# Optimization experiments

Measured on AMD Instinct MI355X. Metric: run time of the kernel, lower is better.

Reference implementation:

```python
import jax, jax.numpy as jnp
import numpy as np

B, CIN, H, W = 8, 128, 64, 64
COUT, KH, KW = 128, 3, 3
STRIDE = (1, 1)
PAD = (1, 1)
DIL = (1, 1)
GROUPS = 1
OFFSET_GROUPS = 1

def _out_size(i, k, s, p, d):
    return (i + 2 * p - d * (k - 1) - 1) // s + 1

HO = _out_size(H, KH, STRIDE[0], PAD[0], DIL[0])
WO = _out_size(W, KW, STRIDE[1], PAD[1], DIL[1])


def setup_inputs() -> dict:
    key = jax.random.key(0)
    k1, k2, k3, k4 = jax.random.split(key, 4)
    x = jax.random.normal(k1, (B, CIN, H, W), jnp.float32)
    offset = jax.random.normal(k2, (B, 2 * OFFSET_GROUPS * KH * KW, HO, WO), jnp.float32)
    fan_in = (CIN // GROUPS) * KH * KW
    bound = 1.0 / np.sqrt(fan_in)
    weight = jax.random.uniform(k3, (COUT, CIN // GROUPS, KH, KW), jnp.float32, -bound, bound)
    bias = jax.random.uniform(k4, (COUT,), jnp.float32, -bound, bound)
    return {"x": x, "offset": offset, "weight": weight, "bias": bias}


def _deform_conv2d(x, offset, weight, bias):
    Bn, Cin, Hi, Wi = x.shape
    K = KH * KW
    Goff, Gw = OFFSET_GROUPS, GROUPS
    Cpg = Cin // Goff

    # base sampling positions (before learned offsets)
    ys = jnp.arange(HO, dtype=jnp.float32) * STRIDE[0] - PAD[0]  # [HO]
    xs = jnp.arange(WO, dtype=jnp.float32) * STRIDE[1] - PAD[1]  # [WO]
    base_y = jnp.repeat(jnp.arange(KH, dtype=jnp.float32) * DIL[0], KW)  # [K]
    base_x = jnp.tile(jnp.arange(KW, dtype=jnp.float32) * DIL[1], KH)    # [K]

    # offsets: channel layout is 2*(g*K + k) + {0: dy, 1: dx}
    off = offset.reshape(Bn, Goff, K, 2, HO, WO)
    py = base_y[None, None, :, None, None] + ys[None, None, None, :, None] + off[:, :, :, 0]  # [B,Goff,K,HO,WO]
    px = base_x[None, None, :, None, None] + xs[None, None, None, None, :] + off[:, :, :, 1]

    y0 = jnp.floor(py)
    x0 = jnp.floor(px)
    ly = py - y0  # fractional weights
    lx = px - x0

    xg = x.reshape(Bn, Goff, Cpg, Hi * Wi)

    def gather_one(img, lin):  # img [Cpg, H*W], lin [K,HO,WO] -> [Cpg,K,HO,WO]
        return img[:, lin]

    gather = jax.vmap(jax.vmap(gather_one))  # over B and Goff

    def corner(yi, xi, w):
        # zero-padding semantics: out-of-bounds corner contributes 0
        mask = (yi >= 0) & (yi < Hi) & (xi >= 0) & (xi < Wi)
        iy = jnp.clip(yi, 0, Hi - 1).astype(jnp.int32)
        ix = jnp.clip(xi, 0, Wi - 1).astype(jnp.int32)
        lin = iy * Wi + ix  # [B,Goff,K,HO,WO]
        wm = (w * mask.astype(x.dtype))[:, :, None]  # broadcast over channel axis
        return gather(xg, lin) * wm  # [B,Goff,Cpg,K,HO,WO]

    val = (corner(y0, x0, (1 - ly) * (1 - lx))
           + corner(y0, x0 + 1, (1 - ly) * lx)
           + corner(y0 + 1, x0, ly * (1 - lx))
           + corner(y0 + 1, x0 + 1, ly * lx))  # [B,Goff,Cpg,K,HO,WO]

    # grouped conv accumulate
    val = val.reshape(Bn, Gw, Cin // Gw, K, HO, WO)
    wg = weight.reshape(Gw, COUT // Gw, Cin // Gw, K)
    out = jnp.einsum('bgckhw,gock->bgohw', val, wg).reshape(Bn, COUT, HO, WO)
    return out + bias[None, :, None, None]


def reference(x, offset, weight, bias):
    return _deform_conv2d(x, offset, weight, bias)
```

## Files before the change

kernel.cpp:

```cpp
#include <hip/hip_runtime.h>

typedef unsigned int   u32;
typedef unsigned short u16;
typedef short bf16x8 __attribute__((ext_vector_type(8)));
typedef float f32x4  __attribute__((ext_vector_type(4)));
typedef float f32x2  __attribute__((ext_vector_type(2)));

#define CIN   128
#define COUT  128
#define Hh    64
#define Ww    64
#define Bb    8
#define NKSTEP 36
#define XT_ELEMS (Bb*Hh*Ww*CIN)

__device__ __forceinline__ float bflo(u32 u){ return __uint_as_float(u << 16); }
__device__ __forceinline__ float bfhi(u32 u){ return __uint_as_float(u & 0xffff0000u); }

__device__ __forceinline__ u32 pack2(float a, float b){
    u32 lo = __float_as_uint(a) + 0x8000u;
    u32 hi = __float_as_uint(b) + 0x8000u;
    return __builtin_amdgcn_perm(hi, lo, 0x07060302u);
}
__device__ __forceinline__ u16 tobf(float a){
    u32 ua = __float_as_uint(a);
    ua += 0x7fffu + ((ua >> 16) & 1u);
    return (u16)(ua >> 16);
}

__global__ __launch_bounds__(256) void k_transpose(const float* __restrict__ x,
                                                   u16* __restrict__ xT){
    __shared__ float lds[64*132];
    int bi = blockIdx.x;
    int hb = bi & 63, b = bi >> 6;
    int tid = threadIdx.x;

    {
        int r = tid >> 1, cq = tid & 1;
        const float* xp = x + ((size_t)(b*128 + r))*4096 + hb*64 + cq*32;
        float4 v[8];
#pragma unroll
        for (int k = 0; k < 8; ++k) v[k] = *(const float4*)(xp + k*4);
        float* dst = lds + (cq*32)*132 + r;
#pragma unroll
        for (int k = 0; k < 8; ++k){
            dst[(k*4+0)*132] = v[k].x;
            dst[(k*4+1)*132] = v[k].y;
            dst[(k*4+2)*132] = v[k].z;
            dst[(k*4+3)*132] = v[k].w;
        }
    }
    __syncthreads();
    {
        int s = tid >> 2, kq = tid & 3;
        const float* src = lds + s*132 + kq*32;
        u32 r16[16];
#pragma unroll
        for (int k = 0; k < 8; ++k){
            float4 v = *(const float4*)(src + k*4);
            r16[k*2  ] = pack2(v.x, v.y);
            r16[k*2+1] = pack2(v.z, v.w);
        }
        u32* dst = (u32*)xT + ((size_t)(b*4096 + hb*64 + s))*64 + kq*16;
#pragma unroll
        for (int k = 0; k < 4; ++k)
            *(uint4*)(dst + k*4) = *(uint4*)&r16[k*4];
    }
}

__global__ __launch_bounds__(256) void k_wprep(const float* __restrict__ w,
                                               u16* __restrict__ Wt){
    int gid = blockIdx.x*256 + threadIdx.x;
    int jf   = gid & 7;
    int lane = (gid >> 3) & 63;
    int mt   = (gid >> 9) & 7;
    int kt   = gid >> 12;
    int m  = mt*16 + (lane & 15);
    int kk = (lane >> 4)*8 + jf;
    int ck = kt*32 + kk;
    int kpos = ck >> 7;
    int cin  = ck & 127;
    Wt[gid] = tobf(w[((size_t)m*128 + cin)*9 + kpos]);
}

__global__ __launch_bounds__(256, 4)
void k_main(const float* __restrict__ off, const float* __restrict__ bias,
            const u16* __restrict__ xT, const u16* __restrict__ Wt,
            float* __restrict__ out){
    __shared__ u32 Vsm[2][32*20];

    int tid = threadIdx.x;
    int bi  = blockIdx.x;
    int b   = bi & 7;
    int t   = bi >> 3;
    int s0  = t * 32;
    int ho  = s0 >> 6, wo0 = s0 & 63;

    int p = tid >> 3, o = tid & 7;
    int wo = wo0 + p;
    const u16* xb = xT + (size_t)b * (Hh*Ww*CIN);

    int lane = tid & 63, wave = tid >> 6;
    int wm = wave >> 1, wn = wave & 1;
    int quad = lane >> 4, l16 = lane & 15;

    f32x4 acc[4];
#pragma unroll
    for (int i = 0; i < 4; ++i) acc[i] = {0.f, 0.f, 0.f, 0.f};

    int   aa[4];
    float wt[4];

    auto state = [&](int kpos){
        int kh = kpos / 3, kw = kpos - kh*3;
        size_t ob = ((size_t)(b*18 + 2*kpos))*4096 + (s0 + p);
        float dy = off[ob];
        float dx = off[ob + 4096];
        float py = (float)(ho + kh - 1) + dy;
        float px = (float)(wo + kw - 1) + dx;
        float y0f = floorf(py), x0f = floorf(px);
        float ly = py - y0f, lx = px - x0f;
        int y0 = (int)y0f, x0 = (int)x0f;
        int y1 = y0 + 1,  x1 = x0 + 1;
        float my0 = (y0 >= 0 && y0 < Hh) ? 1.f : 0.f;
        float my1 = (y1 >= 0 && y1 < Hh) ? 1.f : 0.f;
        float mx0 = (x0 >= 0 && x0 < Ww) ? 1.f : 0.f;
        float mx1 = (x1 >= 0 && x1 < Ww) ? 1.f : 0.f;
        float oy = 1.f - ly, ox = 1.f - lx;
        wt[0] = oy*ox*my0*mx0;
        wt[1] = oy*lx*my0*mx1;
        wt[2] = ly*ox*my1*mx0;
        wt[3] = ly*lx*my1*mx1;
        int cy0 = min(max(y0,0),Hh-1), cy1 = min(max(y1,0),Hh-1);
        int cx0 = min(max(x0,0),Ww-1), cx1 = min(max(x1,0),Ww-1);
        aa[0] = (cy0*Ww + cx0)*CIN;
        aa[1] = (cy0*Ww + cx1)*CIN;
        aa[2] = (cy1*Ww + cx0)*CIN;
        aa[3] = (cy1*Ww + cx1)*CIN;
    };

    auto gather = [&](int ks, uint2 q[4]){
        int coff = ((ks & 3) << 5) + o*4;
        const u16* xc = xb + coff;
#pragma unroll
        for (int c = 0; c < 4; ++c)
            q[c] = *(const uint2*)(xc + aa[c]);
    };

    auto loadA = [&](int ks, uint4 a[4]){
        const u16* wp = Wt + (size_t)((ks*8 + wm*4)*64 + lane)*8;
#pragma unroll
        for (int i = 0; i < 4; ++i)
            a[i] = *(const uint4*)(wp + (size_t)i*64*8);
    };

    auto blend_store = [&](const uint2 q[4], int buf){
        u32 r2[2];
#pragma unroll
        for (int d = 0; d < 2; ++d){
            f32x2 s = {0.f, 0.f};
#pragma unroll
            for (int c = 0; c < 4; ++c){
                u32 u = ((const u32*)q)[c*2 + d];
                f32x2 v  = { bflo(u), bfhi(u) };
                f32x2 w2 = { wt[c], wt[c] };
                s += w2 * v;
            }
            r2[d] = pack2(s.x, s.y);
        }
        *(uint2*)&Vsm[buf][p*20 + o*2] = *(uint2*)&r2[0];
    };

    uint2 q[4];
    uint4 araw_cur[4], araw_nxt[4];
    state(0);
    gather(0, q);
    loadA(0, araw_cur);
    blend_store(q, 0);

    for (int ks = 0; ks < NKSTEP; ++ks){
        __syncthreads();
        int nxt = ks + 1;
        bool have_nxt = (nxt < NKSTEP);
        if (have_nxt){
            if ((nxt & 3) == 0) state(nxt >> 2);
            gather(nxt, q);
            loadA(nxt, araw_nxt);
        }

        uint4 braw = *(const uint4*)&Vsm[ks & 1][(wn*16 + l16)*20 + quad*4];
        bf16x8 bv = __builtin_bit_cast(bf16x8, braw);
#pragma unroll
        for (int i = 0; i < 4; ++i){
            bf16x8 av = __builtin_bit_cast(bf16x8, araw_cur[i]);
            acc[i] = __builtin_amdgcn_mfma_f32_16x16x32_bf16(av, bv, acc[i], 0, 0, 0);
        }

        if (have_nxt){
            blend_store(q, nxt & 1);
#pragma unroll
            for (int i = 0; i < 4; ++i) araw_cur[i] = araw_nxt[i];
        }
    }

    int pcol = wn*16 + l16;
#pragma unroll
    for (int i = 0; i < 4; ++i){
        int cout0 = (wm*4 + i)*16 + quad*4;
        size_t obase = ((size_t)(b*COUT + cout0))*4096 + (s0 + pcol);
#pragma unroll
        for (int r = 0; r < 4; ++r)
            out[obase + (size_t)r*4096] = acc[i][r] + bias[cout0 + r];
    }
}

extern "C" void kernel_launch(void* const* d_in, const int* in_sizes, int n_in,
                              void* d_out, int out_size, void* d_ws, size_t ws_size,
                              hipStream_t stream){
    const float* x    = (const float*)d_in[0];
    const float* off  = (const float*)d_in[1];
    const float* w    = (const float*)d_in[2];
    const float* bias = (const float*)d_in[3];
    float* out = (float*)d_out;

    u16* xT = (u16*)d_ws;
    u16* Wt = xT + XT_ELEMS;

    k_transpose<<<dim3(512),  dim3(256), 0, stream>>>(x, xT);
    k_wprep    <<<dim3(576),  dim3(256), 0, stream>>>(w, Wt);
    k_main     <<<dim3(1024), dim3(256), 0, stream>>>(off, bias, xT, Wt, out);
}
```

Measured before the change: 119.7 us.

## Deepen gather pipeline to two steps ahead and prefetch offsets

```diff
diff --git a/kernel.cpp b/kernel.cpp
--- a/kernel.cpp
+++ b/kernel.cpp
@@ -99,6 +99,7 @@
     int p = tid >> 3, o = tid & 7;
     int wo = wo0 + p;
     const u16* xb = xT + (size_t)b * (Hh*Ww*CIN);
+    const float* offp = off + ((size_t)b*18)*4096 + s0 + p;
 
     int lane = tid & 63, wave = tid >> 6;
     int wm = wave >> 1, wn = wave & 1;
@@ -108,14 +109,19 @@
 #pragma unroll
     for (int i = 0; i < 4; ++i) acc[i] = {0.f, 0.f, 0.f, 0.f};
 
-    int   aa[4];
-    float wt[4];
-
-    auto state = [&](int kpos){
+    int   aaS[2][4];
+    float wtS[2][4];
+    float dyN, dxN;
+
+    auto load_off = [&](int kpos){
+        const float* op = offp + (size_t)(2*kpos)*4096;
+        dyN = op[0];
+        dxN = op[4096];
+    };
+    auto state = [&](int kpos, int st){
+        float dy = dyN, dx = dxN;
+        if (kpos < 8) load_off(kpos + 1);
         int kh = kpos / 3, kw = kpos - kh*3;
-        size_t ob = ((size_t)(b*18 + 2*kpos))*4096 + (s0 + p);
-        float dy = off[ob];
-        float dx = off[ob + 4096];
         float py = (float)(ho + kh - 1) + dy;
         float px = (float)(wo + kw - 1) + dx;
         float y0f = floorf(py), x0f = floorf(px);
@@ -127,34 +133,31 @@
         float mx0 = (x0 >= 0 && x0 < Ww) ? 1.f : 0.f;
         float mx1 = (x1 >= 0 && x1 < Ww) ? 1.f : 0.f;
         float oy = 1.f - ly, ox = 1.f - lx;
-        wt[0] = oy*ox*my0*mx0;
-        wt[1] = oy*lx*my0*mx1;
-        wt[2] = ly*ox*my1*mx0;
-        wt[3] = ly*lx*my1*mx1;
+        wtS[st][0] = oy*ox*my0*mx0;
+        wtS[st][1] = oy*lx*my0*mx1;
+        wtS[st][2] = ly*ox*my1*mx0;
+        wtS[st][3] = ly*lx*my1*mx1;
         int cy0 = min(max(y0,0),Hh-1), cy1 = min(max(y1,0),Hh-1);
         int cx0 = min(max(x0,0),Ww-1), cx1 = min(max(x1,0),Ww-1);
-        aa[0] = (cy0*Ww + cx0)*CIN;
-        aa[1] = (cy0*Ww + cx1)*CIN;
-        aa[2] = (cy1*Ww + cx0)*CIN;
-        aa[3] = (cy1*Ww + cx1)*CIN;
-    };
-
-    auto gather = [&](int ks, uint2 q[4]){
-        int coff = ((ks & 3) << 5) + o*4;
-        const u16* xc = xb + coff;
-#pragma unroll
-        for (int c = 0; c < 4; ++c)
-            q[c] = *(const uint2*)(xc + aa[c]);
-    };
-
-    auto loadA = [&](int ks, uint4 a[4]){
-        const u16* wp = Wt + (size_t)((ks*8 + wm*4)*64 + lane)*8;
+        aaS[st][0] = (cy0*Ww + cx0)*CIN;
+        aaS[st][1] = (cy0*Ww + cx1)*CIN;
+        aaS[st][2] = (cy1*Ww + cx0)*CIN;
+        aaS[st][3] = (cy1*Ww + cx1)*CIN;
+    };
+    auto gather = [&](int c, uint2 q[4]){
+        int st = (c >> 2) & 1;
+        const u16* xc = xb + ((c & 3) << 5) + o*4;
+#pragma unroll
+        for (int cc = 0; cc < 4; ++cc)
+            q[cc] = *(const uint2*)(xc + aaS[st][cc]);
+    };
+    auto loadA = [&](int c, uint4 a[4]){
+        const u16* wp = Wt + (size_t)((c*8 + wm*4)*64 + lane)*8;
 #pragma unroll
         for (int i = 0; i < 4; ++i)
             a[i] = *(const uint4*)(wp + (size_t)i*64*8);
     };
-
-    auto blend_store = [&](const uint2 q[4], int buf){
+    auto blend_store = [&](const uint2 q[4], int st, int buf){
         u32 r2[2];
 #pragma unroll
         for (int d = 0; d < 2; ++d){
@@ -163,7 +166,7 @@
             for (int c = 0; c < 4; ++c){
                 u32 u = ((const u32*)q)[c*2 + d];
                 f32x2 v  = { bflo(u), bfhi(u) };
-                f32x2 w2 = { wt[c], wt[c] };
+                f32x2 w2 = { wtS[st][c], wtS[st][c] };
                 s += w2 * v;
             }
             r2[d] = pack2(s.x, s.y);
@@ -171,36 +174,35 @@
         *(uint2*)&Vsm[buf][p*20 + o*2] = *(uint2*)&r2[0];
     };
 
-    uint2 q[4];
-    uint4 araw_cur[4], araw_nxt[4];
-    state(0);
-    gather(0, q);
-    loadA(0, araw_cur);
-    blend_store(q, 0);
-
+    uint2 qb[2][4];
+    uint4 av[2][4];
+    load_off(0);
+    state(0, 0);
+    gather(0, qb[0]);
+    loadA(0, av[0]);
+    blend_store(qb[0], 0, 0);
+    gather(1, qb[1]);
+
+#pragma unroll
     for (int ks = 0; ks < NKSTEP; ++ks){
         __syncthreads();
-        int nxt = ks + 1;
-        bool have_nxt = (nxt < NKSTEP);
-        if (have_nxt){
-            if ((nxt & 3) == 0) state(nxt >> 2);
-            gather(nxt, q);
-            loadA(nxt, araw_nxt);
-        }
+        int c1 = ks + 1, c2 = ks + 2;
+        if (c2 < NKSTEP){
+            if ((c2 & 3) == 0) state(c2 >> 2, (c2 >> 2) & 1);
+            gather(c2, qb[ks & 1]);
+        }
+        if (c1 < NKSTEP) loadA(c1, av[c1 & 1]);
 
         uint4 braw = *(const uint4*)&Vsm[ks & 1][(wn*16 + l16)*20 + quad*4];
         bf16x8 bv = __builtin_bit_cast(bf16x8, braw);
 #pragma unroll
         for (int i = 0; i < 4; ++i){
-            bf16x8 av = __builtin_bit_cast(bf16x8, araw_cur[i]);
-            acc[i] = __builtin_amdgcn_mfma_f32_16x16x32_bf16(av, bv, acc[i], 0, 0, 0);
-        }
-
-        if (have_nxt){
-            blend_store(q, nxt & 1);
-#pragma unroll
-            for (int i = 0; i < 4; ++i) araw_cur[i] = araw_nxt[i];
-        }
+            bf16x8 avv = __builtin_bit_cast(bf16x8, av[ks & 1][i]);
+            acc[i] = __builtin_amdgcn_mfma_f32_16x16x32_bf16(avv, bv, acc[i], 0, 0, 0);
+        }
+
+        if (c1 < NKSTEP)
+            blend_store(qb[c1 & 1], (c1 >> 2) & 1, c1 & 1);
     }
 
     int pcol = wn*16 + l16;
```

Result: no change. 118.3 us (-1.1%).
